# Kernel tuning notes

Measured on AMD Instinct MI355X. Metric: run time of the kernel, lower is better.

The kernel has to match this reference:

```python
import jax, jax.numpy as jnp
import numpy as np

N = 100000      # num_assets (nodes)
E = 1600000     # edges (avg degree 16)
D_IN, D_H, D_OUT = 128, 64, 64


def gcn_conv(x, W, b, src, dst, dinv):
    """PyG-style GCNConv: h = D^{-1/2}(A+I)D^{-1/2} (x @ W) + b.
    Self-loop contribution handled analytically (norm = dinv[i]^2)."""
    h = x @ W                                   # [N, out]
    norm = dinv[src] * dinv[dst]                # [E]
    agg = jax.ops.segment_sum(h[src] * norm[:, None], dst, num_segments=N)
    agg = agg + h * (dinv * dinv)[:, None]      # self-loops
    return agg + b


def setup_inputs() -> dict:
    key = jax.random.key(0)
    ks = jax.random.split(key, 10)
    x = jax.random.normal(ks[0], (N, D_IN), dtype=jnp.float32)
    edge_index = jax.random.randint(ks[1], (2, E), 0, N, dtype=jnp.int64)
    s = 0.1
    W1 = jax.random.normal(ks[2], (D_IN, D_H), dtype=jnp.float32) * s
    b1 = jnp.zeros((D_H,), dtype=jnp.float32)
    W2 = jax.random.normal(ks[3], (D_H, D_H), dtype=jnp.float32) * s
    b2 = jnp.zeros((D_H,), dtype=jnp.float32)
    W3 = jax.random.normal(ks[4], (D_H, D_OUT), dtype=jnp.float32) * s
    b3 = jnp.zeros((D_OUT,), dtype=jnp.float32)
    Wa = jax.random.normal(ks[5], (D_OUT, D_OUT), dtype=jnp.float32) * s  # torch Linear weight [out,in]
    ba = jnp.zeros((D_OUT,), dtype=jnp.float32)
    q = jax.random.normal(ks[6], (D_OUT, 1), dtype=jnp.float32)
    battn = jax.random.normal(ks[7], (1,), dtype=jnp.float32)
    return {"x": x, "edge_index": edge_index, "W1": W1, "b1": b1,
            "W2": W2, "b2": b2, "W3": W3, "b3": b3,
            "Wa": Wa, "ba": ba, "q": q, "battn": battn}


def reference(x, edge_index, W1, b1, W2, b2, W3, b3, Wa, ba, q, battn):
    src, dst = edge_index[0], edge_index[1]
    # degree of A + I (computed once, shared by all layers)
    deg = jax.ops.segment_sum(jnp.ones((E,), dtype=x.dtype), dst, num_segments=N) + 1.0
    dinv = jax.lax.rsqrt(deg)

    h = jax.nn.relu(gcn_conv(x, W1, b1, src, dst, dinv))
    h = jax.nn.relu(gcn_conv(h, W2, b2, src, dst, dinv))
    z_context = gcn_conv(h, W3, b3, src, dst, dinv)          # [N, D_OUT]

    attn_scores = jnp.tanh(z_context @ Wa.T + ba) @ q + battn  # [N, 1]
    attn = jax.nn.softmax(attn_scores, axis=0)                 # softmax over nodes
    global_context = jnp.sum(attn * z_context, axis=0)         # [D_OUT]
    return (z_context, global_context)
```

## Files before the change

kernel.cpp:

```cpp
#include <hip/hip_runtime.h>
#include <hip/hip_fp16.h>
#include <math.h>
#include <stdint.h>


__global__ void detect_i64_kernel(const int* __restrict__ ei, int* __restrict__ flag) {
    int t = threadIdx.x;
    int bad = 0;
#pragma unroll
    for (int j = 0; j < 4; j++)
        bad |= (ei[1 + 2 * (t * 4 + j)] != 0);
    unsigned long long m = __ballot(bad);
    if (t == 0) *flag = (m == 0ull) ? 1 : 0;
}

__global__ void fill_kernel(const void* __restrict__ ei, const int* __restrict__ flag,
                            int* __restrict__ cnt, int* __restrict__ buckets,
                            int CAP, int E, int lo, int hi) {
    int e = blockIdx.x * 256 + threadIdx.x;
    if (e >= E) return;
    int is64 = *flag;
    int d = is64 ? (int)((const long long*)ei)[E + e] : ((const int*)ei)[E + e];
    if (d < lo || d >= hi) return;
    int s = is64 ? (int)((const long long*)ei)[e] : ((const int*)ei)[e];
    int pos = atomicAdd(&cnt[d], 1);
    if (pos < CAP) buckets[(size_t)d * CAP + pos] = s;
}

__global__ void dinv_kernel(const int* __restrict__ cnt, float* __restrict__ dinv, int N) {
    int i = blockIdx.x * 256 + threadIdx.x;
    if (i < N) dinv[i] = rsqrtf((float)cnt[i] + 1.0f);
}

template <int K, bool PRE>
__global__ __launch_bounds__(256) void gemm64(const float* __restrict__ in,
                                              const float* __restrict__ Wg,
                                              const float* __restrict__ bias,
                                              const float* __restrict__ dinv,
                                              __half* __restrict__ outh, int nrows) {
    constexpr int KQ = K / 4;
    __shared__ float Wl[K * 64];
    __shared__ float bl[K];
    const int t  = threadIdx.x;
    const int rb = blockIdx.x * 64;

    for (int idx = t; idx < K * 16; idx += 256)
        *(float4*)(Wl + idx * 4) = *(const float4*)(Wg + idx * 4);
    if (PRE) {
        for (int idx = t; idx < K; idx += 256) bl[idx] = bias[idx];
    }
    __syncthreads();

    const int tc = t & 15;
    const int tr = t >> 4;
    int rowi[4];
#pragma unroll
    for (int i = 0; i < 4; i++) {
        int r = rb + tr * 4 + i;
        rowi[i] = (r < nrows) ? r : (nrows - 1);
    }

    float acc[4][4];
#pragma unroll
    for (int i = 0; i < 4; i++)
#pragma unroll
        for (int j = 0; j < 4; j++) acc[i][j] = 0.f;

#pragma unroll 2
    for (int kb = 0; kb < KQ; ++kb) {
        float4 a[4];
#pragma unroll
        for (int i = 0; i < 4; i++)
            a[i] = *(const float4*)(in + (size_t)rowi[i] * K + (kb << 2));
        if (PRE) {
            float4 bb = *(const float4*)(bl + (kb << 2));
#pragma unroll
            for (int i = 0; i < 4; i++) {
                a[i].x = fmaxf(a[i].x + bb.x, 0.f);
                a[i].y = fmaxf(a[i].y + bb.y, 0.f);
                a[i].z = fmaxf(a[i].z + bb.z, 0.f);
                a[i].w = fmaxf(a[i].w + bb.w, 0.f);
            }
        }
        float4 w0 = *(const float4*)(Wl + ((kb << 2) + 0) * 64 + tc * 4);
        float4 w1 = *(const float4*)(Wl + ((kb << 2) + 1) * 64 + tc * 4);
        float4 w2 = *(const float4*)(Wl + ((kb << 2) + 2) * 64 + tc * 4);
        float4 w3 = *(const float4*)(Wl + ((kb << 2) + 3) * 64 + tc * 4);
#pragma unroll
        for (int i = 0; i < 4; i++) {
            acc[i][0] += a[i].x * w0.x + a[i].y * w1.x + a[i].z * w2.x + a[i].w * w3.x;
            acc[i][1] += a[i].x * w0.y + a[i].y * w1.y + a[i].z * w2.y + a[i].w * w3.y;
            acc[i][2] += a[i].x * w0.z + a[i].y * w1.z + a[i].z * w2.z + a[i].w * w3.z;
            acc[i][3] += a[i].x * w0.w + a[i].y * w1.w + a[i].z * w2.w + a[i].w * w3.w;
        }
    }
#pragma unroll
    for (int i = 0; i < 4; i++) {
        int r = rb + tr * 4 + i;
        if (r < nrows) {
            float dd = dinv[r];
            __half2 p0 = __floats2half2_rn(acc[i][0] * dd, acc[i][1] * dd);
            __half2 p1 = __floats2half2_rn(acc[i][2] * dd, acc[i][3] * dd);
            uint2 pk;
            pk.x = *(unsigned int*)&p0;
            pk.y = *(unsigned int*)&p1;
            *(uint2*)(outh + (size_t)r * 64 + tc * 4) = pk;
        }
    }
}

template <bool BIAS>
__global__ __launch_bounds__(256) void gather64(const __half* __restrict__ hs,
                                                const int* __restrict__ cnt,
                                                const int* __restrict__ buckets,
                                                int CAP,
                                                const float* __restrict__ bias,
                                                float* __restrict__ out, int N) {
    const int wid = (blockIdx.x * 256 + threadIdx.x) >> 6;
    if (wid >= N) return;
    const int lane = threadIdx.x & 63;
    const int g    = lane >> 4;
    const int q    = lane & 15;

    const int deg  = cnt[wid];
    const int degc = min(deg, CAP);
    const int* bk  = buckets + (size_t)wid * CAP;
    const int pm   = degc - 1;

    float4 acc = make_float4(0.f, 0.f, 0.f, 0.f);
    if (g == 0) {
        uint2 v = *(const uint2*)(hs + (size_t)wid * 64 + q * 4);
        float2 f0 = __half22float2(*(__half2*)&v.x);
        float2 f1 = __half22float2(*(__half2*)&v.y);
        acc = make_float4(f0.x, f0.y, f1.x, f1.y);
    }

    for (int base = 0; base < degc; base += 16) {
        int i0 = base + g;
        int i1 = i0 + 4;
        int i2 = i0 + 8;
        int i3 = i0 + 12;
        int s0 = bk[i0 <= pm ? i0 : pm];
        int s1 = bk[i1 <= pm ? i1 : pm];
        int s2 = bk[i2 <= pm ? i2 : pm];
        int s3 = bk[i3 <= pm ? i3 : pm];
        uint2 v0 = *(const uint2*)(hs + (size_t)s0 * 64 + q * 4);
        uint2 v1 = *(const uint2*)(hs + (size_t)s1 * 64 + q * 4);
        uint2 v2 = *(const uint2*)(hs + (size_t)s2 * 64 + q * 4);
        uint2 v3 = *(const uint2*)(hs + (size_t)s3 * 64 + q * 4);
        float m0 = (i0 <= pm) ? 1.f : 0.f;
        float m1 = (i1 <= pm) ? 1.f : 0.f;
        float m2 = (i2 <= pm) ? 1.f : 0.f;
        float m3 = (i3 <= pm) ? 1.f : 0.f;
        float2 a0 = __half22float2(*(__half2*)&v0.x), b0 = __half22float2(*(__half2*)&v0.y);
        float2 a1 = __half22float2(*(__half2*)&v1.x), b1 = __half22float2(*(__half2*)&v1.y);
        float2 a2 = __half22float2(*(__half2*)&v2.x), b2 = __half22float2(*(__half2*)&v2.y);
        float2 a3 = __half22float2(*(__half2*)&v3.x), b3 = __half22float2(*(__half2*)&v3.y);
        acc.x = fmaf(m0, a0.x, acc.x); acc.y = fmaf(m0, a0.y, acc.y);
        acc.z = fmaf(m0, b0.x, acc.z); acc.w = fmaf(m0, b0.y, acc.w);
        acc.x = fmaf(m1, a1.x, acc.x); acc.y = fmaf(m1, a1.y, acc.y);
        acc.z = fmaf(m1, b1.x, acc.z); acc.w = fmaf(m1, b1.y, acc.w);
        acc.x = fmaf(m2, a2.x, acc.x); acc.y = fmaf(m2, a2.y, acc.y);
        acc.z = fmaf(m2, b2.x, acc.z); acc.w = fmaf(m2, b2.y, acc.w);
        acc.x = fmaf(m3, a3.x, acc.x); acc.y = fmaf(m3, a3.y, acc.y);
        acc.z = fmaf(m3, b3.x, acc.z); acc.w = fmaf(m3, b3.y, acc.w);
    }
    acc.x += __shfl_xor(acc.x, 16); acc.y += __shfl_xor(acc.y, 16);
    acc.z += __shfl_xor(acc.z, 16); acc.w += __shfl_xor(acc.w, 16);
    acc.x += __shfl_xor(acc.x, 32); acc.y += __shfl_xor(acc.y, 32);
    acc.z += __shfl_xor(acc.z, 32); acc.w += __shfl_xor(acc.w, 32);

    if (g == 0) {
        float dd = rsqrtf((float)deg + 1.0f);
        float4 o = make_float4(acc.x * dd, acc.y * dd, acc.z * dd, acc.w * dd);
        if (BIAS) {
            float4 b = *(const float4*)(bias + q * 4);
            o.x += b.x; o.y += b.y; o.z += b.z; o.w += b.w;
        }
        *(float4*)(out + (size_t)wid * 64 + q * 4) = o;
    }
}

__device__ __forceinline__ float fast_tanh(float x) {
    float e = __expf(2.f * x);
    return 1.f - 2.f * __builtin_amdgcn_rcpf(e + 1.f);
}

__global__ __launch_bounds__(64) void scoregc_kernel(const float* __restrict__ z,
                                                     const float* __restrict__ Wa,
                                                     const float* __restrict__ ba,
                                                     const float* __restrict__ q,
                                                     const float* __restrict__ battn,
                                                     float* __restrict__ blockmax,
                                                     float* __restrict__ bsumE,
                                                     float* __restrict__ bpart, int N) {
    const int t = threadIdx.x;
    const int i = blockIdx.x * 64 + t;
    const bool act = (i < N);

    float zi[64];
    if (act) {
#pragma unroll
        for (int kq = 0; kq < 16; kq++) {
            float4 v = *(const float4*)(z + (size_t)i * 64 + kq * 4);
            zi[kq * 4 + 0] = v.x; zi[kq * 4 + 1] = v.y;
            zi[kq * 4 + 2] = v.z; zi[kq * 4 + 3] = v.w;
        }
    } else {
#pragma unroll
        for (int k = 0; k < 64; k++) zi[k] = 0.f;
    }

    float sc = -1e30f;
    {
        float s = battn[0];
        for (int j = 0; j < 64; j++) {
            float t0 = ba[j], t1 = 0.f, t2 = 0.f, t3 = 0.f;
#pragma unroll
            for (int kq = 0; kq < 16; kq++) {
                float4 w4 = *(const float4*)(Wa + j * 64 + kq * 4);
                t0 = fmaf(zi[kq * 4 + 0], w4.x, t0);
                t1 = fmaf(zi[kq * 4 + 1], w4.y, t1);
                t2 = fmaf(zi[kq * 4 + 2], w4.z, t2);
                t3 = fmaf(zi[kq * 4 + 3], w4.w, t3);
            }
            s += fast_tanh((t0 + t1) + (t2 + t3)) * q[j];
        }
        if (act) sc = s;
    }

    float m = sc;
#pragma unroll
    for (int off = 32; off > 0; off >>= 1) m = fmaxf(m, __shfl_xor(m, off));
    float e = act ? __expf(sc - m) : 0.f;
    float se = e;
#pragma unroll
    for (int off = 32; off > 0; off >>= 1) se += __shfl_xor(se, off);
    if (t == 0) { blockmax[blockIdx.x] = m; bsumE[blockIdx.x] = se; }

    const int base = blockIdx.x * 64;
    float a = 0.f;
    for (int n = 0; n < 64; n++) {
        float en = __shfl(e, n);
        int idx = base + n;
        idx = (idx < N) ? idx : (N - 1);
        a = fmaf(en, z[(size_t)idx * 64 + t], a);
    }
    bpart[(size_t)blockIdx.x * 64 + t] = a;
}

__global__ __launch_bounds__(1024) void final3_kernel(const float* __restrict__ blockmax,
                                                      const float* __restrict__ bsumE,
                                                      const float* __restrict__ bpart,
                                                      int NB, float* __restrict__ outg) {
    __shared__ float sm[1024];
    __shared__ float se[1024];
    __shared__ float sa[16][64];
    int t = threadIdx.x;
    float m = -1e30f;
    for (int b = t; b < NB; b += 1024) m = fmaxf(m, blockmax[b]);
    sm[t] = m;
    __syncthreads();
    for (int off = 512; off > 0; off >>= 1) {
        if (t < off) sm[t] = fmaxf(sm[t], sm[t + off]);
        __syncthreads();
    }
    float M = sm[0];

    float es = 0.f;
    for (int b = t; b < NB; b += 1024) es += bsumE[b] * __expf(blockmax[b] - M);
    se[t] = es;
    __syncthreads();
    for (int off = 512; off > 0; off >>= 1) {
        if (t < off) se[t] += se[t + off];
        __syncthreads();
    }

    int f = t & 63, c = t >> 6;
    float a = 0.f;
    for (int b = c; b < NB; b += 16)
        a += bpart[(size_t)b * 64 + f] * __expf(blockmax[b] - M);
    sa[c][f] = a;
    __syncthreads();
    for (int off = 8; off > 0; off >>= 1) {
        if (c < off) sa[c][f] += sa[c + off][f];
        __syncthreads();
    }
    if (c == 0) outg[f] = sa[0][f] / se[0];
}

extern "C" void kernel_launch(void* const* d_in, const int* in_sizes, int n_in,
                              void* d_out, int out_size, void* d_ws, size_t ws_size,
                              hipStream_t stream) {
    const float* x     = (const float*)d_in[0];
    const void*  ei    = d_in[1];
    const float* W1    = (const float*)d_in[2];
    const float* b1    = (const float*)d_in[3];
    const float* W2    = (const float*)d_in[4];
    const float* b2    = (const float*)d_in[5];
    const float* W3    = (const float*)d_in[6];
    const float* b3    = (const float*)d_in[7];
    const float* Wa    = (const float*)d_in[8];
    const float* ba    = (const float*)d_in[9];
    const float* q     = (const float*)d_in[10];
    const float* battn = (const float*)d_in[11];

    const int N = in_sizes[0] / 128;
    const int E = in_sizes[1] / 2;

    float*  ws       = (float*)d_ws;
    float*  dinv     = ws;
    __half* H        = (__half*)(ws + N);
    float*  blockmax = ws + N + (size_t)32 * N;
    float*  bsumE    = blockmax + 2048;
    float*  bpart    = bsumE + 2048;
    int*    flag     = (int*)(bpart + 2048 * 64);
    int*    cnt      = flag + 4;
    int*    buckets  = cnt + N;

    size_t fixed_bytes = (size_t)((char*)buckets - (char*)d_ws);
    size_t rem = (ws_size > fixed_bytes) ? (ws_size - fixed_bytes) : 0;
    size_t cap_fit = rem / ((size_t)N * sizeof(int));
    int CAP = (int)(cap_fit < 64 ? cap_fit : 64);
    if (CAP < 8) CAP = 8;

    float* Z    = (float*)d_out;
    float* outg = Z + (size_t)N * 64;

    hipMemsetAsync(cnt, 0, (size_t)N * sizeof(int), stream);
    detect_i64_kernel<<<1, 64, 0, stream>>>((const int*)ei, flag);

    const int NP = 2;
    const int rng = (N + NP - 1) / NP;
    for (int p = 0; p < NP; ++p) {
        int lo = p * rng;
        int hi = (p == NP - 1) ? N : lo + rng;
        fill_kernel<<<(E + 255) / 256, 256, 0, stream>>>(ei, flag, cnt, buckets,
                                                         CAP, E, lo, hi);
    }
    dinv_kernel<<<(N + 255) / 256, 256, 0, stream>>>(cnt, dinv, N);

    const int gb = (N + 63) / 64;
    const int ag = (int)(((long long)N * 64 + 255) / 256);
    const int NBW = (N + 63) / 64;

    gemm64<128, false><<<gb, 256, 0, stream>>>(x, W1, nullptr, dinv, H, N);
    gather64<false><<<ag, 256, 0, stream>>>(H, cnt, buckets, CAP, nullptr, Z, N);

    gemm64<64, true><<<gb, 256, 0, stream>>>(Z, W2, b1, dinv, H, N);
    gather64<false><<<ag, 256, 0, stream>>>(H, cnt, buckets, CAP, nullptr, Z, N);

    gemm64<64, true><<<gb, 256, 0, stream>>>(Z, W3, b2, dinv, H, N);
    gather64<true><<<ag, 256, 0, stream>>>(H, cnt, buckets, CAP, b3, Z, N);

    scoregc_kernel<<<NBW, 64, 0, stream>>>(Z, Wa, ba, q, battn,
                                           blockmax, bsumE, bpart, N);
    final3_kernel<<<1, 1024, 0, stream>>>(blockmax, bsumE, bpart, NBW, outg);
}
```

Measured before the change: 381.7 us.

## Fuse neighbor gather with next-layer GEMM in a persistent wave kernel

Replaces the separate gather→fp32 Z→gemm sequence for layers 2 and 3 with a persistent kernel. Each wave aggregates a node's neighbors, applies bias and ReLU, then multiplies by the next weight matrix held in registers, using lane shuffles to broadcast the aggregated row. It writes the half-precision pre-scaled result directly, using the output buffer as scratch. This removes the fp32 intermediate write/read and two launches, at the cost of 64 registers of weights per thread and 64 shuffles per node. The fill pass is also split into four destination ranges instead of two.

New measurement: 418.9 us. +9.7%, slower.

```diff
diff --git a/kernel.cpp b/kernel.cpp
--- a/kernel.cpp
+++ b/kernel.cpp
@@ -109,24 +109,10 @@
     }
 }
 
-template <bool BIAS>
-__global__ __launch_bounds__(256) void gather64(const __half* __restrict__ hs,
-                                                const int* __restrict__ cnt,
-                                                const int* __restrict__ buckets,
-                                                int CAP,
-                                                const float* __restrict__ bias,
-                                                float* __restrict__ out, int N) {
-    const int wid = (blockIdx.x * 256 + threadIdx.x) >> 6;
-    if (wid >= N) return;
-    const int lane = threadIdx.x & 63;
-    const int g    = lane >> 4;
-    const int q    = lane & 15;
-
-    const int deg  = cnt[wid];
-    const int degc = min(deg, CAP);
-    const int* bk  = buckets + (size_t)wid * CAP;
-    const int pm   = degc - 1;
-
+__device__ __forceinline__ float4 gather_acc(const __half* __restrict__ hs,
+                                             const int* __restrict__ bk,
+                                             int wid, int degc, int g, int q) {
+    const int pm = degc - 1;
     float4 acc = make_float4(0.f, 0.f, 0.f, 0.f);
     if (g == 0) {
         uint2 v = *(const uint2*)(hs + (size_t)wid * 64 + q * 4);
@@ -134,7 +120,6 @@
         float2 f1 = __half22float2(*(__half2*)&v.y);
         acc = make_float4(f0.x, f0.y, f1.x, f1.y);
     }
-
     for (int base = 0; base < degc; base += 16) {
         int i0 = base + g;
         int i1 = i0 + 4;
@@ -169,15 +154,69 @@
     acc.z += __shfl_xor(acc.z, 16); acc.w += __shfl_xor(acc.w, 16);
     acc.x += __shfl_xor(acc.x, 32); acc.y += __shfl_xor(acc.y, 32);
     acc.z += __shfl_xor(acc.z, 32); acc.w += __shfl_xor(acc.w, 32);
-
+    return acc;
+}
+
+__global__ __launch_bounds__(256) void gather64(const __half* __restrict__ hs,
+                                                const int* __restrict__ cnt,
+                                                const int* __restrict__ buckets,
+                                                int CAP,
+                                                const float* __restrict__ bias,
+                                                float* __restrict__ out, int N) {
+    const int wid = (blockIdx.x * 256 + threadIdx.x) >> 6;
+    if (wid >= N) return;
+    const int lane = threadIdx.x & 63;
+    const int g = lane >> 4, q = lane & 15;
+    const int deg  = cnt[wid];
+    const int degc = min(deg, CAP);
+    float4 acc = gather_acc(hs, buckets + (size_t)wid * CAP, wid, degc, g, q);
     if (g == 0) {
         float dd = rsqrtf((float)deg + 1.0f);
-        float4 o = make_float4(acc.x * dd, acc.y * dd, acc.z * dd, acc.w * dd);
-        if (BIAS) {
-            float4 b = *(const float4*)(bias + q * 4);
-            o.x += b.x; o.y += b.y; o.z += b.z; o.w += b.w;
-        }
+        float4 b = *(const float4*)(bias + q * 4);
+        float4 o = make_float4(fmaf(acc.x, dd, b.x), fmaf(acc.y, dd, b.y),
+                               fmaf(acc.z, dd, b.z), fmaf(acc.w, dd, b.w));
         *(float4*)(out + (size_t)wid * 64 + q * 4) = o;
+    }
+}
+
+__global__ __launch_bounds__(256) void gathergemm_kernel(const __half* __restrict__ hs,
+                                                         const int* __restrict__ cnt,
+                                                         const int* __restrict__ buckets,
+                                                         int CAP,
+                                                         const float* __restrict__ bc,
+                                                         const float* __restrict__ Wn,
+                                                         __half* __restrict__ out, int N) {
+    const int lane = threadIdx.x & 63;
+    const int g = lane >> 4, q = lane & 15;
+
+    float wcol[64];
+#pragma unroll
+    for (int k = 0; k < 64; k++) wcol[k] = Wn[k * 64 + lane];
+    const float4 bq = *(const float4*)(bc + q * 4);
+
+    const int nwaves = gridDim.x * 4;
+    for (int wid = (blockIdx.x * 256 + threadIdx.x) >> 6; wid < N; wid += nwaves) {
+        const int deg  = cnt[wid];
+        const int degc = min(deg, CAP);
+        float4 acc = gather_acc(hs, buckets + (size_t)wid * CAP, wid, degc, g, q);
+        float dd = rsqrtf((float)deg + 1.0f);
+        float a0 = fmaxf(fmaf(acc.x, dd, bq.x), 0.f);
+        float a1 = fmaxf(fmaf(acc.y, dd, bq.y), 0.f);
+        float a2 = fmaxf(fmaf(acc.z, dd, bq.z), 0.f);
+        float a3 = fmaxf(fmaf(acc.w, dd, bq.w), 0.f);
+        float oc = 0.f;
+#pragma unroll
+        for (int kq = 0; kq < 16; kq++) {
+            float ax = __shfl(a0, kq);
+            float ay = __shfl(a1, kq);
+            float az = __shfl(a2, kq);
+            float aw = __shfl(a3, kq);
+            oc = fmaf(ax, wcol[4 * kq + 0],
+                 fmaf(ay, wcol[4 * kq + 1],
+                 fmaf(az, wcol[4 * kq + 2],
+                 fmaf(aw, wcol[4 * kq + 3], oc))));
+        }
+        out[(size_t)wid * 64 + lane] = __float2half(oc * dd);
     }
 }
 
@@ -310,7 +349,7 @@
 
     float*  ws       = (float*)d_ws;
     float*  dinv     = ws;
-    __half* H        = (__half*)(ws + N);
+    __half* H1       = (__half*)(ws + N);
     float*  blockmax = ws + N + (size_t)32 * N;
     float*  bsumE    = blockmax + 2048;
     float*  bpart    = bsumE + 2048;
@@ -324,13 +363,14 @@
     int CAP = (int)(cap_fit < 64 ? cap_fit : 64);
     if (CAP < 8) CAP = 8;
 
-    float* Z    = (float*)d_out;
-    float* outg = Z + (size_t)N * 64;
+    float*  Z    = (float*)d_out;
+    float*  outg = Z + (size_t)N * 64;
+    __half* H2   = (__half*)d_out;
 
     hipMemsetAsync(cnt, 0, (size_t)N * sizeof(int), stream);
     detect_i64_kernel<<<1, 64, 0, stream>>>((const int*)ei, flag);
 
-    const int NP = 2;
+    const int NP = 4;
     const int rng = (N + NP - 1) / NP;
     for (int p = 0; p < NP; ++p) {
         int lo = p * rng;
@@ -343,15 +383,12 @@
     const int gb = (N + 63) / 64;
     const int ag = (int)(((long long)N * 64 + 255) / 256);
     const int NBW = (N + 63) / 64;
-
-    gemm64<128, false><<<gb, 256, 0, stream>>>(x, W1, nullptr, dinv, H, N);
-    gather64<false><<<ag, 256, 0, stream>>>(H, cnt, buckets, CAP, nullptr, Z, N);
-
-    gemm64<64, true><<<gb, 256, 0, stream>>>(Z, W2, b1, dinv, H, N);
-    gather64<false><<<ag, 256, 0, stream>>>(H, cnt, buckets, CAP, nullptr, Z, N);
-
-    gemm64<64, true><<<gb, 256, 0, stream>>>(Z, W3, b2, dinv, H, N);
-    gather64<true><<<ag, 256, 0, stream>>>(H, cnt, buckets, CAP, b3, Z, N);
+    const int fg = 4096;
+
+    gemm64<128, false><<<gb, 256, 0, stream>>>(x, W1, nullptr, dinv, H1, N);
+    gathergemm_kernel<<<fg, 256, 0, stream>>>(H1, cnt, buckets, CAP, b1, W2, H2, N);
+    gathergemm_kernel<<<fg, 256, 0, stream>>>(H2, cnt, buckets, CAP, b2, W3, H1, N);
+    gather64<<<ag, 256, 0, stream>>>(H1, cnt, buckets, CAP, b3, Z, N);
 
     scoregc_kernel<<<NBW, 64, 0, stream>>>(Z, Wa, ba, q, battn,
                                            blockmax, bsumE, bpart, N);
```
